# Optimization experiments

Hardware: AMD Instinct MI355X
Metric: run time of the kernel (lower is better)

The kernel has to match this reference:

```python
import jax, jax.numpy as jnp
import numpy as np


def setup_inputs() -> dict:
    key = jax.random.key(0)
    ks = jax.random.split(key, 8)
    N, E, F_IN, H, OUT = 20000, 320000, 386, 256, 2
    x = jax.random.normal(ks[0], (N, F_IN), dtype=jnp.float32)
    src = jax.random.randint(ks[1], (E,), 0, N)
    dst = jax.random.randint(ks[2], (E,), 0, N)
    W1 = jax.random.normal(ks[3], (F_IN, H), dtype=jnp.float32) / np.sqrt(F_IN)
    b1 = jnp.zeros((H,), dtype=jnp.float32)
    W2 = jax.random.normal(ks[4], (H, OUT), dtype=jnp.float32) / np.sqrt(H)
    b2 = jnp.zeros((OUT,), dtype=jnp.float32)
    return {"x": x, "src": src, "dst": dst, "W1": W1, "b1": b1, "W2": W2, "b2": b2}


def reference(x, src, dst, W1, b1, W2, b2):
    N = x.shape[0]
    # PyG GCNConv: add self-loops, deg from destination (col), sym normalization
    deg = jnp.ones((N,), x.dtype).at[dst].add(1.0)  # self-loop + in-degree
    dis = deg ** -0.5                                # deg^{-1/2}
    edge_norm = dis[src] * dis[dst]                  # [E]
    self_norm = dis * dis                            # [N] (self-loop weight)

    def gcn_conv(h, W, b):
        h = h @ W                                    # [N, F_out] transform first
        msgs = h[src] * edge_norm[:, None]           # [E, F_out] gathered messages
        agg = jax.ops.segment_sum(msgs, dst, num_segments=N)
        agg = agg + h * self_norm[:, None]           # self-loop contribution
        return agg + b

    h = jax.nn.relu(gcn_conv(x, W1, b1))
    out = gcn_conv(h, W2, b2)
    return jnp.tanh(out)
```

## Files before the change

### kernel.cpp

```cpp
#include <hip/hip_runtime.h>
#include <math.h>

typedef _Float16 f16;
typedef _Float16 f16x8 __attribute__((ext_vector_type(8)));
typedef float f32x4 __attribute__((ext_vector_type(4)));

#define FIN 386
#define KP  416
#define HH  256
#define ELLW 64
#define NP  20032

#define GBM 64
#define GBN 128
#define GBK 32


__global__ __launch_bounds__(256) void k_prep(
    int* __restrict__ cursor, int N,
    const float* __restrict__ W1, f16* __restrict__ wt,
    const float* __restrict__ x, f16* __restrict__ xh) {
    int i = blockIdx.x * 256 + threadIdx.x;
    if (i < N) cursor[i] = 0;
    if (i < HH * KP) {
        int c = i / KP, k = i - c * KP;
        wt[i] = (k < FIN) ? (f16)W1[(size_t)k * HH + c] : (f16)0.f;
    }
    const int CPR = KP / 8;
    if (i < NP * CPR) {
        int row = i / CPR;
        int k2 = (i - row * CPR) * 8;
        f16x8 t = {};
        if (row < N && k2 < FIN) {
            const float* p = x + (size_t)row * FIN + k2;
            if (k2 + 8 <= FIN) {
                float2 f0 = *(const float2*)(p);
                float2 f1 = *(const float2*)(p + 2);
                float2 f2 = *(const float2*)(p + 4);
                float2 f3 = *(const float2*)(p + 6);
                t[0] = (f16)f0.x; t[1] = (f16)f0.y;
                t[2] = (f16)f1.x; t[3] = (f16)f1.y;
                t[4] = (f16)f2.x; t[5] = (f16)f2.y;
                t[6] = (f16)f3.x; t[7] = (f16)f3.y;
            } else {
                #pragma unroll
                for (int j = 0; j < 8; ++j)
                    t[j] = (k2 + j < FIN) ? (f16)p[j] : (f16)0.f;
            }
        }
        *(f16x8*)(xh + (size_t)row * KP + k2) = t;
    }
}


__global__ __launch_bounds__(256) void k_mid(
    const f16* __restrict__ A, const f16* __restrict__ Bt,
    f16* __restrict__ C, int nbg,
    const int* __restrict__ src, const int* __restrict__ dst,
    int* __restrict__ cursor, int* __restrict__ ell, int E, int nbf) {

    if ((int)blockIdx.x >= nbg) {
        for (int e = ((int)blockIdx.x - nbg) * 256 + threadIdx.x; e < E; e += nbf * 256) {
            int s = src[e], d = dst[e];
            int slot = atomicAdd(&cursor[d], 1);
            if (slot < ELLW) ell[(size_t)d * ELLW + slot] = s;
        }
        return;
    }

    const int gb = blockIdx.x;
    const int bm = (gb >> 1) * GBM;
    const int bn = (gb & 1) * GBN;
    const int tid = threadIdx.x;
    const int w = tid >> 6, l = tid & 63;
    const int wr = (w & 1) * 32;
    const int wc = (w >> 1) * 64;
    const int lrow = l & 15, lslot = l >> 4;

    const f16* pa0 = A  + (size_t)(bm + wr + lrow) * KP + lslot * 8;
    const f16* pa1 = pa0 + (size_t)16 * KP;
    const f16* pb  = Bt + (size_t)(bn + wc + lrow) * KP + lslot * 8;

    f32x4 acc[2][4] = {};

    #pragma unroll
    for (int k0 = 0; k0 < KP; k0 += GBK) {
        f16x8 a0 = *(const f16x8*)(pa0 + k0);
        f16x8 a1 = *(const f16x8*)(pa1 + k0);
        f16x8 b0 = *(const f16x8*)(pb + k0);
        f16x8 b1 = *(const f16x8*)(pb + (size_t)16 * KP + k0);
        f16x8 b2 = *(const f16x8*)(pb + (size_t)32 * KP + k0);
        f16x8 b3 = *(const f16x8*)(pb + (size_t)48 * KP + k0);
        acc[0][0] = __builtin_amdgcn_mfma_f32_16x16x32_f16(a0, b0, acc[0][0], 0, 0, 0);
        acc[1][0] = __builtin_amdgcn_mfma_f32_16x16x32_f16(a1, b0, acc[1][0], 0, 0, 0);
        acc[0][1] = __builtin_amdgcn_mfma_f32_16x16x32_f16(a0, b1, acc[0][1], 0, 0, 0);
        acc[1][1] = __builtin_amdgcn_mfma_f32_16x16x32_f16(a1, b1, acc[1][1], 0, 0, 0);
        acc[0][2] = __builtin_amdgcn_mfma_f32_16x16x32_f16(a0, b2, acc[0][2], 0, 0, 0);
        acc[1][2] = __builtin_amdgcn_mfma_f32_16x16x32_f16(a1, b2, acc[1][2], 0, 0, 0);
        acc[0][3] = __builtin_amdgcn_mfma_f32_16x16x32_f16(a0, b3, acc[0][3], 0, 0, 0);
        acc[1][3] = __builtin_amdgcn_mfma_f32_16x16x32_f16(a1, b3, acc[1][3], 0, 0, 0);
    }

    #pragma unroll
    for (int mi = 0; mi < 2; ++mi) {
        #pragma unroll
        for (int r = 0; r < 4; ++r) {
            int row = bm + wr + mi * 16 + lslot * 4 + r;
            #pragma unroll
            for (int ni = 0; ni < 4; ++ni)
                C[(size_t)row * HH + bn + wc + ni * 16 + lrow] = (f16)acc[mi][ni][r];
        }
    }
}


__global__ __launch_bounds__(256) void k_agg1(
    const f16* __restrict__ h1h, const int* __restrict__ ell,
    const int* __restrict__ cursor, const float* __restrict__ b1,
    const float* __restrict__ W2, float* __restrict__ z, int N) {
    const int sl = threadIdx.x & 31;
    const int d = blockIdx.x * 8 + (threadIdx.x >> 5);
    if (d >= N) return;

    const float4* bp = (const float4*)b1 + sl * 2;
    const float4 bb0 = bp[0], bb1 = bp[1];
    const float4* wp = (const float4*)W2 + sl * 4;
    const float4 wv0 = wp[0], wv1 = wp[1], wv2 = wp[2], wv3 = wp[3];

    int cd = cursor[d];
    float dd = rsqrtf((float)(cd + 1));
    int cnt = cd > ELLW ? ELLW : cd;
    const int* erow = ell + (size_t)d * ELLW;

    f16x8 v = ((const f16x8*)(h1h + (size_t)d * HH))[sl];
    float e[8];
    #pragma unroll
    for (int i = 0; i < 8; ++i) e[i] = dd * (float)v[i];

    int j = 0;
    for (; j + 3 < cnt; j += 4) {
        int s0 = erow[j], s1 = erow[j + 1], s2 = erow[j + 2], s3 = erow[j + 3];
        float u0 = rsqrtf((float)(cursor[s0] + 1));
        float u1 = rsqrtf((float)(cursor[s1] + 1));
        float u2 = rsqrtf((float)(cursor[s2] + 1));
        float u3 = rsqrtf((float)(cursor[s3] + 1));
        f16x8 q0 = ((const f16x8*)(h1h + (size_t)s0 * HH))[sl];
        f16x8 q1 = ((const f16x8*)(h1h + (size_t)s1 * HH))[sl];
        f16x8 q2 = ((const f16x8*)(h1h + (size_t)s2 * HH))[sl];
        f16x8 q3 = ((const f16x8*)(h1h + (size_t)s3 * HH))[sl];
        #pragma unroll
        for (int i = 0; i < 8; ++i)
            e[i] += u0 * (float)q0[i] + u1 * (float)q1[i]
                  + u2 * (float)q2[i] + u3 * (float)q3[i];
    }
    for (; j < cnt; ++j) {
        int s0 = erow[j];
        float u0 = rsqrtf((float)(cursor[s0] + 1));
        f16x8 q0 = ((const f16x8*)(h1h + (size_t)s0 * HH))[sl];
        #pragma unroll
        for (int i = 0; i < 8; ++i) e[i] += u0 * (float)q0[i];
    }

    float a[8];
    a[0] = fmaxf(dd * e[0] + bb0.x, 0.0f);
    a[1] = fmaxf(dd * e[1] + bb0.y, 0.0f);
    a[2] = fmaxf(dd * e[2] + bb0.z, 0.0f);
    a[3] = fmaxf(dd * e[3] + bb0.w, 0.0f);
    a[4] = fmaxf(dd * e[4] + bb1.x, 0.0f);
    a[5] = fmaxf(dd * e[5] + bb1.y, 0.0f);
    a[6] = fmaxf(dd * e[6] + bb1.z, 0.0f);
    a[7] = fmaxf(dd * e[7] + bb1.w, 0.0f);

    float p0 = a[0] * wv0.x + a[1] * wv0.z + a[2] * wv1.x + a[3] * wv1.z
             + a[4] * wv2.x + a[5] * wv2.z + a[6] * wv3.x + a[7] * wv3.z;
    float p1 = a[0] * wv0.y + a[1] * wv0.w + a[2] * wv1.y + a[3] * wv1.w
             + a[4] * wv2.y + a[5] * wv2.w + a[6] * wv3.y + a[7] * wv3.w;
    #pragma unroll
    for (int off = 16; off > 0; off >>= 1) {
        p0 += __shfl_down(p0, off, 32);
        p1 += __shfl_down(p1, off, 32);
    }
    if (sl == 0)
        *(float2*)(z + 2 * (size_t)d) = make_float2(p0, p1);
}


__global__ __launch_bounds__(256) void k_agg2(
    const float* __restrict__ z, const int* __restrict__ ell,
    const int* __restrict__ cursor, const float* __restrict__ b2,
    float* __restrict__ out, int N) {
    int d = blockIdx.x * 256 + threadIdx.x;
    if (d >= N) return;
    const float c0 = b2[0], c1 = b2[1];
    int cd = cursor[d];
    float dd = rsqrtf((float)(cd + 1));
    int cnt = cd > ELLW ? ELLW : cd;
    const int* erow = ell + (size_t)d * ELLW;
    float2 zz = *(const float2*)(z + 2 * (size_t)d);
    float e0 = dd * zz.x, e1 = dd * zz.y;
    int j = 0;
    for (; j + 3 < cnt; j += 4) {
        int s0 = erow[j], s1 = erow[j + 1], s2 = erow[j + 2], s3 = erow[j + 3];
        float u0 = rsqrtf((float)(cursor[s0] + 1));
        float u1 = rsqrtf((float)(cursor[s1] + 1));
        float u2 = rsqrtf((float)(cursor[s2] + 1));
        float u3 = rsqrtf((float)(cursor[s3] + 1));
        float2 z0 = *(const float2*)(z + 2 * (size_t)s0);
        float2 z1 = *(const float2*)(z + 2 * (size_t)s1);
        float2 z2 = *(const float2*)(z + 2 * (size_t)s2);
        float2 z3 = *(const float2*)(z + 2 * (size_t)s3);
        e0 += u0 * z0.x + u1 * z1.x + u2 * z2.x + u3 * z3.x;
        e1 += u0 * z0.y + u1 * z1.y + u2 * z2.y + u3 * z3.y;
    }
    for (; j < cnt; ++j) {
        int s = erow[j];
        float u = rsqrtf((float)(cursor[s] + 1));
        float2 zv = *(const float2*)(z + 2 * (size_t)s);
        e0 += u * zv.x;
        e1 += u * zv.y;
    }
    out[d * 2 + 0] = tanhf(dd * e0 + c0);
    out[d * 2 + 1] = tanhf(dd * e1 + c1);
}


extern "C" void kernel_launch(void* const* d_in, const int* in_sizes, int n_in,
                              void* d_out, int out_size, void* d_ws, size_t ws_size,
                              hipStream_t stream) {
    const float* x   = (const float*)d_in[0];
    const int*   src = (const int*)d_in[1];
    const int*   dst = (const int*)d_in[2];
    const float* W1  = (const float*)d_in[3];
    const float* b1  = (const float*)d_in[4];
    const float* W2  = (const float*)d_in[5];
    const float* b2  = (const float*)d_in[6];
    float* out = (float*)d_out;

    const int E = in_sizes[1];
    const int N = in_sizes[0] / FIN;

    char* base = (char*)d_ws;
    size_t off = 0;
    f16* wt     = (f16*)(base + off); off += (size_t)HH * KP * sizeof(f16);
    f16* xh     = (f16*)(base + off); off += (size_t)NP * KP * sizeof(f16);
    f16* h1h    = (f16*)(base + off); off += (size_t)NP * HH * sizeof(f16);
    int* ell    = (int*)(base + off); off += (size_t)N * ELLW * sizeof(int);
    float* z    = (float*)(base + off); off += 2 * (size_t)N * sizeof(float);
    int* cursor = (int*)(base + off); off += (size_t)N * sizeof(int);

    const int T = 256;
    const int CPR = KP / 8;
    int prep_work = NP * CPR;
    const int nbg = (NP / GBM) * (HH / GBN);
    const int nbf = 512;

    k_prep<<<(prep_work + T - 1) / T, T, 0, stream>>>(cursor, N, W1, wt, x, xh);
    k_mid<<<nbg + nbf, T, 0, stream>>>(xh, wt, h1h, nbg, src, dst, cursor, ell, E, nbf);
    k_agg1<<<(N + 7) / 8, T, 0, stream>>>(h1h, ell, cursor, b1, W2, z, N);
    k_agg2<<<(N + T - 1) / T, T, 0, stream>>>(z, ell, cursor, b2, out, N);
}
```

Measured before the change: 71.64 us.

## Fuse fp32-to-fp16 conversion of x into the GEMM A-operand loads

The separate pass that converted x to a padded fp16 buffer is removed. The GEMM now reads fp32 rows of x directly and converts them in registers, handling the last partial K chunk (columns 384–385) specially and clamping out-of-range rows to row 0. This removes the write and later re-read of a roughly 16 MB intermediate and shrinks the prep kernel. In exchange, the GEMM loads twice as many bytes per A element, and each x row is fetched by both column-half blocks.

```diff
diff --git a/kernel.cpp b/kernel.cpp
--- a/kernel.cpp
+++ b/kernel.cpp
@@ -18,44 +18,32 @@
 
 __global__ __launch_bounds__(256) void k_prep(
     int* __restrict__ cursor, int N,
-    const float* __restrict__ W1, f16* __restrict__ wt,
-    const float* __restrict__ x, f16* __restrict__ xh) {
+    const float* __restrict__ W1, f16* __restrict__ wt) {
     int i = blockIdx.x * 256 + threadIdx.x;
     if (i < N) cursor[i] = 0;
     if (i < HH * KP) {
         int c = i / KP, k = i - c * KP;
         wt[i] = (k < FIN) ? (f16)W1[(size_t)k * HH + c] : (f16)0.f;
     }
-    const int CPR = KP / 8;
-    if (i < NP * CPR) {
-        int row = i / CPR;
-        int k2 = (i - row * CPR) * 8;
-        f16x8 t = {};
-        if (row < N && k2 < FIN) {
-            const float* p = x + (size_t)row * FIN + k2;
-            if (k2 + 8 <= FIN) {
-                float2 f0 = *(const float2*)(p);
-                float2 f1 = *(const float2*)(p + 2);
-                float2 f2 = *(const float2*)(p + 4);
-                float2 f3 = *(const float2*)(p + 6);
-                t[0] = (f16)f0.x; t[1] = (f16)f0.y;
-                t[2] = (f16)f1.x; t[3] = (f16)f1.y;
-                t[4] = (f16)f2.x; t[5] = (f16)f2.y;
-                t[6] = (f16)f3.x; t[7] = (f16)f3.y;
-            } else {
-                #pragma unroll
-                for (int j = 0; j < 8; ++j)
-                    t[j] = (k2 + j < FIN) ? (f16)p[j] : (f16)0.f;
-            }
-        }
-        *(f16x8*)(xh + (size_t)row * KP + k2) = t;
-    }
+}
+
+__device__ __forceinline__ f16x8 lda8(const float* p) {
+    float2 f0 = *(const float2*)(p);
+    float2 f1 = *(const float2*)(p + 2);
+    float2 f2 = *(const float2*)(p + 4);
+    float2 f3 = *(const float2*)(p + 6);
+    f16x8 t;
+    t[0] = (f16)f0.x; t[1] = (f16)f0.y;
+    t[2] = (f16)f1.x; t[3] = (f16)f1.y;
+    t[4] = (f16)f2.x; t[5] = (f16)f2.y;
+    t[6] = (f16)f3.x; t[7] = (f16)f3.y;
+    return t;
 }
 
 
 __global__ __launch_bounds__(256) void k_mid(
-    const f16* __restrict__ A, const f16* __restrict__ Bt,
-    f16* __restrict__ C, int nbg,
+    const float* __restrict__ X, const f16* __restrict__ Bt,
+    f16* __restrict__ C, int nbg, int N,
     const int* __restrict__ src, const int* __restrict__ dst,
     int* __restrict__ cursor, int* __restrict__ ell, int E, int nbf) {
 
@@ -77,16 +65,42 @@
     const int wc = (w >> 1) * 64;
     const int lrow = l & 15, lslot = l >> 4;
 
-    const f16* pa0 = A  + (size_t)(bm + wr + lrow) * KP + lslot * 8;
-    const f16* pa1 = pa0 + (size_t)16 * KP;
-    const f16* pb  = Bt + (size_t)(bn + wc + lrow) * KP + lslot * 8;
+    int ar0 = bm + wr + lrow;       if (ar0 >= N) ar0 = 0;
+    int ar1 = bm + wr + 16 + lrow;  if (ar1 >= N) ar1 = 0;
+
+    const float* pa0 = X + (size_t)ar0 * FIN + lslot * 8;
+    const float* pa1 = X + (size_t)ar1 * FIN + lslot * 8;
+    const f16*   pb  = Bt + (size_t)(bn + wc + lrow) * KP + lslot * 8;
 
     f32x4 acc[2][4] = {};
 
     #pragma unroll
-    for (int k0 = 0; k0 < KP; k0 += GBK) {
-        f16x8 a0 = *(const f16x8*)(pa0 + k0);
-        f16x8 a1 = *(const f16x8*)(pa1 + k0);
+    for (int k0 = 0; k0 < 12 * GBK; k0 += GBK) {
+        f16x8 a0 = lda8(pa0 + k0);
+        f16x8 a1 = lda8(pa1 + k0);
+        f16x8 b0 = *(const f16x8*)(pb + k0);
+        f16x8 b1 = *(const f16x8*)(pb + (size_t)16 * KP + k0);
+        f16x8 b2 = *(const f16x8*)(pb + (size_t)32 * KP + k0);
+        f16x8 b3 = *(const f16x8*)(pb + (size_t)48 * KP + k0);
+        acc[0][0] = __builtin_amdgcn_mfma_f32_16x16x32_f16(a0, b0, acc[0][0], 0, 0, 0);
+        acc[1][0] = __builtin_amdgcn_mfma_f32_16x16x32_f16(a1, b0, acc[1][0], 0, 0, 0);
+        acc[0][1] = __builtin_amdgcn_mfma_f32_16x16x32_f16(a0, b1, acc[0][1], 0, 0, 0);
+        acc[1][1] = __builtin_amdgcn_mfma_f32_16x16x32_f16(a1, b1, acc[1][1], 0, 0, 0);
+        acc[0][2] = __builtin_amdgcn_mfma_f32_16x16x32_f16(a0, b2, acc[0][2], 0, 0, 0);
+        acc[1][2] = __builtin_amdgcn_mfma_f32_16x16x32_f16(a1, b2, acc[1][2], 0, 0, 0);
+        acc[0][3] = __builtin_amdgcn_mfma_f32_16x16x32_f16(a0, b3, acc[0][3], 0, 0, 0);
+        acc[1][3] = __builtin_amdgcn_mfma_f32_16x16x32_f16(a1, b3, acc[1][3], 0, 0, 0);
+    }
+
+    {
+        const int k0 = 384;
+        f16x8 a0 = {}, a1 = {};
+        if (lslot == 0) {
+            float2 f0 = *(const float2*)(pa0 + k0);
+            float2 f1 = *(const float2*)(pa1 + k0);
+            a0[0] = (f16)f0.x; a0[1] = (f16)f0.y;
+            a1[0] = (f16)f1.x; a1[1] = (f16)f1.y;
+        }
         f16x8 b0 = *(const f16x8*)(pb + k0);
         f16x8 b1 = *(const f16x8*)(pb + (size_t)16 * KP + k0);
         f16x8 b2 = *(const f16x8*)(pb + (size_t)32 * KP + k0);
@@ -242,20 +256,18 @@
     char* base = (char*)d_ws;
     size_t off = 0;
     f16* wt     = (f16*)(base + off); off += (size_t)HH * KP * sizeof(f16);
-    f16* xh     = (f16*)(base + off); off += (size_t)NP * KP * sizeof(f16);
     f16* h1h    = (f16*)(base + off); off += (size_t)NP * HH * sizeof(f16);
     int* ell    = (int*)(base + off); off += (size_t)N * ELLW * sizeof(int);
     float* z    = (float*)(base + off); off += 2 * (size_t)N * sizeof(float);
     int* cursor = (int*)(base + off); off += (size_t)N * sizeof(int);
 
     const int T = 256;
-    const int CPR = KP / 8;
-    int prep_work = NP * CPR;
+    const int prep_work = HH * KP;
     const int nbg = (NP / GBM) * (HH / GBN);
     const int nbf = 512;
 
-    k_prep<<<(prep_work + T - 1) / T, T, 0, stream>>>(cursor, N, W1, wt, x, xh);
-    k_mid<<<nbg + nbf, T, 0, stream>>>(xh, wt, h1h, nbg, src, dst, cursor, ell, E, nbf);
+    k_prep<<<(prep_work + T - 1) / T, T, 0, stream>>>(cursor, N, W1, wt);
+    k_mid<<<nbg + nbf, T, 0, stream>>>(x, wt, h1h, nbg, N, src, dst, cursor, ell, E, nbf);
     k_agg1<<<(N + 7) / 8, T, 0, stream>>>(h1h, ell, cursor, b1, W2, z, N);
     k_agg2<<<(N + T - 1) / T, T, 0, stream>>>(z, ell, cursor, b2, out, N);
 }
```

New measurement: 74.51 us. 4.0% more time.
